# Optimization experiments

Measured on AMD Instinct MI355X. Metric: run time of the kernel, lower is better.

The kernel has to match this reference:

```python
import jax, jax.numpy as jnp
import numpy as np

N_RBF = 20
CUTOFF = 15.0
N_ATOMS, N_EDGES, D, H = 8192, 262144, 256, 256
D_PAIR = 2 * D + 1 + N_RBF  # 533


def setup_inputs() -> dict:
    key = jax.random.key(0)
    ks = jax.random.split(key, 10)
    s = 1.0 / np.sqrt(H).astype(np.float32)
    return {
        "x": jax.random.normal(ks[0], (N_ATOMS, D), jnp.float32),
        "d_ij": jax.random.uniform(ks[1], (N_EDGES,), jnp.float32, 0.5, CUTOFF),
        "idx_i": jnp.sort(jax.random.randint(ks[2], (N_EDGES,), 0, N_ATOMS)),
        "idx_j": jax.random.randint(ks[3], (N_EDGES,), 0, N_ATOMS),
        "W_in": jax.random.normal(ks[4], (D_PAIR, H), jnp.float32) / np.sqrt(D_PAIR).astype(np.float32),
        "b_in": jnp.zeros((H,), jnp.float32),
        "Ws": jax.random.normal(ks[5], (6, H, H), jnp.float32) * s,
        "bs": jnp.zeros((6, H), jnp.float32),
        "W_out": jax.random.normal(ks[6], (H, 1), jnp.float32) * s,
        "b_out": jnp.zeros((1,), jnp.float32),
    }


def _gaussian_rbf(d):
    # GaussianRBF(20, 15.0): offsets linspace(0, cutoff), width = grid spacing
    offsets = jnp.linspace(0.0, CUTOFF, N_RBF)
    width = offsets[1] - offsets[0]
    coeff = -0.5 / (width * width)
    diff = d[:, None] - offsets  # [E, N_RBF]
    return jnp.exp(coeff * diff * diff)


def reference(x, d_ij, idx_i, idx_j, W_in, b_in, Ws, bs, W_out, b_out):
    n_atoms = x.shape[0]
    rbf = _gaussian_rbf(d_ij)  # [E, 20]
    # per-pair representation: x_i | x_j | rbf(d_ij) | d_ij  -> [E, 533]
    pair = jnp.concatenate([x[idx_i], x[idx_j], rbf, d_ij[:, None]], axis=1)
    h = pair @ W_in + b_in  # pair_and_distance_transform -> [E, 256]
    # build_mlp(H, H, H, 5): 6 linears, SiLU after all but the last
    for l in range(6):
        h = h @ Ws[l] + bs[l]
        if l < 5:
            h = jax.nn.silu(h)
    # DeepSets aggregation: scatter-sum pair messages onto center atom i
    pooled = jax.ops.segment_sum(h, idx_i, num_segments=n_atoms)  # [N, 256]
    out = pooled @ W_out + b_out  # per-atom energy [N, 1]
    return out
```

## Files before the change

kernel.cpp:

```cpp
#include <hip/hip_runtime.h>


typedef _Float16 f16x8 __attribute__((ext_vector_type(8)));
typedef _Float16 f16x4 __attribute__((ext_vector_type(4)));
typedef __fp16   fp16v2 __attribute__((ext_vector_type(2)));
typedef float    f32x4 __attribute__((ext_vector_type(4)));
typedef unsigned int u32x4 __attribute__((ext_vector_type(4)));
typedef unsigned int u32x2 __attribute__((ext_vector_type(2)));

union H8 { f16x8 v; _Float16 h[8]; u32x4 u; };
union H4 { f16x4 v; u32x2 u; };
union H2 { fp16v2 h; unsigned int u; };

#define MFMA16(a, b, c) __builtin_amdgcn_mfma_f32_16x16x32_f16((a), (b), (c), 0, 0, 0)

#define LOG2E 1.44269504088896340736f

#define WS_WP   0u
#define WS_WPI  786432u
#define WS_WPJ  917504u
#define WS_WPR  1048576u
#define WS_XH   1064960u
#define WS_AP   5259264u
#define WS_BP   9453568u

__global__ __launch_bounds__(256) void k_prep(
    const float* __restrict__ x, const float* __restrict__ W_in,
    const float* __restrict__ Ws, const float* __restrict__ b_out,
    _Float16* __restrict__ wp, _Float16* __restrict__ wpi,
    _Float16* __restrict__ wpj, _Float16* __restrict__ wpr,
    _Float16* __restrict__ xh, float* __restrict__ out)
{
  int i = blockIdx.x * 256 + threadIdx.x;
  if (i < 2097152) { xh[i] = (_Float16)x[i]; return; }
  i -= 2097152;
  if (i < 393216) {
    int m = i >> 16, r = i & 65535;
    int j = r & 7, lane = (r >> 3) & 63, ks = (r >> 9) & 7, nt = (r >> 12) & 15;
    int k = ks * 32 + (lane >> 4) * 8 + j, n = nt * 16 + (lane & 15);
    wp[i] = (_Float16)Ws[(m * 256 + k) * 256 + n];
    return;
  }
  i -= 393216;
  if (i < 65536) {
    int j = i & 7, lane = (i >> 3) & 63, ks = (i >> 9) & 7, nt = (i >> 12) & 15;
    int k = ks * 32 + (lane >> 4) * 8 + j, n = nt * 16 + (lane & 15);
    wpi[i] = (_Float16)W_in[k * 256 + n];
    return;
  }
  i -= 65536;
  if (i < 65536) {
    int j = i & 7, lane = (i >> 3) & 63, ks = (i >> 9) & 7, nt = (i >> 12) & 15;
    int k = ks * 32 + (lane >> 4) * 8 + j, n = nt * 16 + (lane & 15);
    wpj[i] = (_Float16)W_in[(256 + k) * 256 + n];
    return;
  }
  i -= 65536;
  if (i < 8192) {
    int j = i & 7, lane = (i >> 3) & 63, nt = (i >> 9) & 15;
    int k = (lane >> 4) * 8 + j, n = nt * 16 + (lane & 15);
    float v = 0.0f;
    if (k < 20)       v = W_in[(512 + k) * 256 + n];
    else if (k == 20) v = W_in[532 * 256 + n];
    wpr[i] = (_Float16)v;
    return;
  }
  i -= 8192;
  if (i < 8192) out[i] = b_out[0];
}

__global__ __launch_bounds__(256) void k_atoms(
    const _Float16* __restrict__ xh,
    const _Float16* __restrict__ wpi, const _Float16* __restrict__ wpj,
    const float* __restrict__ b_in,
    _Float16* __restrict__ AP, _Float16* __restrict__ BP)
{
  const int tid = threadIdx.x;
  const int l = tid & 63, w = tid >> 6;
  const int g = l >> 4, c = l & 15;
  const int which = blockIdx.y;
  const _Float16* wpx = which ? wpj : wpi;
  _Float16* outp = which ? BP : AP;
  const int abase = blockIdx.x * 64;

  f32x4 acc[4][4];
#pragma unroll
  for (int nf = 0; nf < 4; ++nf)
#pragma unroll
    for (int at = 0; at < 4; ++at) acc[nf][at] = (f32x4)0.0f;

#pragma unroll
  for (int ks = 0; ks < 8; ++ks) {
    f16x8 a[4];
#pragma unroll
    for (int nf = 0; nf < 4; ++nf) {
      H8 t; t.u = *(const u32x4*)(wpx + (((w * 4 + nf) * 8 + ks) * 64 + l) * 8);
      a[nf] = t.v;
    }
#pragma unroll
    for (int at = 0; at < 4; ++at) {
      H8 b; b.u = *(const u32x4*)(xh + (abase + at * 16 + c) * 256 + ks * 32 + g * 8);
#pragma unroll
      for (int nf = 0; nf < 4; ++nf)
        acc[nf][at] = MFMA16(a[nf], b.v, acc[nf][at]);
    }
  }

#pragma unroll
  for (int nf = 0; nf < 4; ++nf) {
    const int n = w * 64 + nf * 16 + g * 4;
    f32x4 bias = (f32x4)0.0f;
    if (!which) bias = *(const f32x4*)(b_in + n);
#pragma unroll
    for (int at = 0; at < 4; ++at) {
      const int atom = abase + at * 16 + c;
      const f32x4 t = acc[nf][at] + bias;
      H2 lo, hi;
      lo.h = __builtin_amdgcn_cvt_pkrtz(t[0], t[1]);
      hi.h = __builtin_amdgcn_cvt_pkrtz(t[2], t[3]);
      u32x2 q; q[0] = lo.u; q[1] = hi.u;
      *(u32x2*)(outp + atom * 256 + n) = q;
    }
  }
}

__global__ __launch_bounds__(512, 2) void k_edges(
    const _Float16* __restrict__ AP, const _Float16* __restrict__ BP,
    const int* __restrict__ idx_i, const int* __restrict__ idx_j,
    const float* __restrict__ d_ij,
    const _Float16* __restrict__ wp, const _Float16* __restrict__ wpr,
    const float* __restrict__ bs, const float* __restrict__ W_out,
    float* __restrict__ out)
{
  __shared__ __align__(16) char hb[131072];
  __shared__ float d_lds[256];
  __shared__ int   ii_lds[256];
  __shared__ int   jj_lds[256];
  __shared__ float oacc[256];

  const int tid = threadIdx.x;
  const int l = tid & 63, w = tid >> 6;
  const int fg = w & 3, eg = w >> 2;
  const int g = l >> 4, c = l & 15;
  const int ebase = blockIdx.x * 256;
  const int nb = fg * 64;
  const int eb = eg * 128;
  const int sw = (c << 4) | ((c & 1) << 8);

  if (tid < 256) {
    ii_lds[tid] = idx_i[ebase + tid];
    jj_lds[tid] = idx_j[ebase + tid];
    d_lds[tid]  = d_ij[ebase + tid];
    oacc[tid]   = 0.0f;
  }
  __syncthreads();

  f32x4 acc[4][8];

  {
    const float STEP = 15.0f / 19.0f;
    const float C2 = (-0.5f / (STEP * STEP)) * LOG2E;
    f16x8 afr[4];
#pragma unroll
    for (int nf = 0; nf < 4; ++nf) {
      H8 t; t.u = *(const u32x4*)(wpr + ((fg * 4 + nf) * 64 + l) * 8);
      afr[nf] = t.v;
    }
#pragma unroll
    for (int et = 0; et < 8; ++et) {
      const float d = d_lds[eb + et * 16 + c];
      H8 bb;
#pragma unroll
      for (int j = 0; j < 8; ++j) {
        const int k = g * 8 + j;
        float v = 0.0f;
        if (k < 20)       { const float df = d - (float)k * STEP; v = __builtin_amdgcn_exp2f(C2 * df * df); }
        else if (k == 20) { v = d; }
        bb.h[j] = (_Float16)v;
      }
      const f32x4 z = (f32x4)0.0f;
#pragma unroll
      for (int nf = 0; nf < 4; ++nf)
        acc[nf][et] = MFMA16(afr[nf], bb.v, z);
    }
  }
#pragma unroll
  for (int nf = 0; nf < 4; ++nf) {
    const int n = nb + nf * 16 + g * 4;
    const int obase = n * 2;
#pragma unroll
    for (int et = 0; et < 8; ++et) {
      const int el = eb + et * 16 + c;
      H4 pa, pb, s;
      pa.u = *(const u32x2*)(AP + ii_lds[el] * 256 + n);
      pb.u = *(const u32x2*)(BP + jj_lds[el] * 256 + n);
      H2 lo, hi;
      lo.h = __builtin_amdgcn_cvt_pkrtz(acc[nf][et][0], acc[nf][et][1]);
      hi.h = __builtin_amdgcn_cvt_pkrtz(acc[nf][et][2], acc[nf][et][3]);
      s.u[0] = lo.u; s.u[1] = hi.u;
      s.v = s.v + pa.v + pb.v;
      *(u32x2*)(hb + el * 512 + (obase ^ sw)) = s.u;
    }
  }
  __syncthreads();

  auto mfma_layer = [&](const _Float16* wl, const float* brow) {
#pragma unroll
    for (int nf = 0; nf < 4; ++nf) {
      const f32x4 bias = *(const f32x4*)(brow + nb + nf * 16 + g * 4);
#pragma unroll
      for (int et = 0; et < 8; ++et) acc[nf][et] = bias;
    }
    __builtin_amdgcn_s_setprio(1);
#pragma unroll
    for (int ks = 0; ks < 8; ++ks) {
      f16x8 a[4];
#pragma unroll
      for (int nf = 0; nf < 4; ++nf) {
        H8 t; t.u = *(const u32x4*)(wl + (((fg * 4 + nf) * 8 + ks) * 64 + l) * 8);
        a[nf] = t.v;
      }
      const int o = (ks * 64 + g * 16) ^ sw;
#pragma unroll
      for (int et = 0; et < 8; ++et) {
        const int el = eb + et * 16 + c;
        H8 b; b.u = *(const u32x4*)(hb + el * 512 + o);
#pragma unroll
        for (int nf = 0; nf < 4; ++nf)
          acc[nf][et] = MFMA16(a[nf], b.v, acc[nf][et]);
      }
    }
    __builtin_amdgcn_s_setprio(0);
  };

#pragma unroll 1
  for (int ly = 0; ly < 5; ++ly) {
    mfma_layer(wp + ly * 65536, bs + ly * 256);
    __syncthreads();
#pragma unroll
    for (int nf = 0; nf < 4; ++nf) {
      const int n = nb + nf * 16 + g * 4;
      const int obase = n * 2;
#pragma unroll
      for (int et = 0; et < 8; ++et) {
        f32x4 v = acc[nf][et];
#pragma unroll
        for (int j = 0; j < 4; ++j) {
          const float e = __builtin_amdgcn_exp2f(v[j] * -LOG2E);
          v[j] = v[j] * __builtin_amdgcn_rcpf(1.0f + e);
        }
        const int el = eb + et * 16 + c;
        H2 lo, hi;
        lo.h = __builtin_amdgcn_cvt_pkrtz(v[0], v[1]);
        hi.h = __builtin_amdgcn_cvt_pkrtz(v[2], v[3]);
        u32x2 q; q[0] = lo.u; q[1] = hi.u;
        *(u32x2*)(hb + el * 512 + (obase ^ sw)) = q;
      }
    }
    __syncthreads();
  }

  mfma_layer(wp + 5 * 65536, bs + 5 * 256);
  float sum[8];
#pragma unroll
  for (int et = 0; et < 8; ++et) sum[et] = 0.0f;
#pragma unroll
  for (int nf = 0; nf < 4; ++nf) {
    const int n = nb + nf * 16 + g * 4;
    const f32x4 wo = *(const f32x4*)(W_out + n);
#pragma unroll
    for (int et = 0; et < 8; ++et) {
      const f32x4 v = acc[nf][et];
      sum[et] += v[0] * wo[0] + v[1] * wo[1] + v[2] * wo[2] + v[3] * wo[3];
    }
  }
#pragma unroll
  for (int et = 0; et < 8; ++et) {
    float s = sum[et];
    s += __shfl_xor(s, 16, 64);
    s += __shfl_xor(s, 32, 64);
    if (l < 16) atomicAdd(&oacc[eb + et * 16 + l], s);
  }
  __syncthreads();
  if (tid < 256) atomicAdd(out + ii_lds[tid], oacc[tid]);
}

extern "C" void kernel_launch(void* const* d_in, const int* in_sizes, int n_in,
                              void* d_out, int out_size, void* d_ws, size_t ws_size,
                              hipStream_t stream) {
  (void)in_sizes; (void)n_in; (void)out_size; (void)ws_size;
  const float* x     = (const float*)d_in[0];
  const float* d_ij  = (const float*)d_in[1];
  const int*   idx_i = (const int*)d_in[2];
  const int*   idx_j = (const int*)d_in[3];
  const float* W_in  = (const float*)d_in[4];
  const float* b_in  = (const float*)d_in[5];
  const float* Ws    = (const float*)d_in[6];
  const float* bs    = (const float*)d_in[7];
  const float* W_out = (const float*)d_in[8];
  const float* b_out = (const float*)d_in[9];
  float* out = (float*)d_out;
  char* ws = (char*)d_ws;

  _Float16* wp  = (_Float16*)(ws + WS_WP);
  _Float16* wpi = (_Float16*)(ws + WS_WPI);
  _Float16* wpj = (_Float16*)(ws + WS_WPJ);
  _Float16* wpr = (_Float16*)(ws + WS_WPR);
  _Float16* xh  = (_Float16*)(ws + WS_XH);
  _Float16* AP  = (_Float16*)(ws + WS_AP);
  _Float16* BP  = (_Float16*)(ws + WS_BP);

  hipLaunchKernelGGL(k_prep, dim3(10305), dim3(256), 0, stream,
                     x, W_in, Ws, b_out, wp, wpi, wpj, wpr, xh, out);
  hipLaunchKernelGGL(k_atoms, dim3(128, 2), dim3(256), 0, stream,
                     xh, wpi, wpj, b_in, AP, BP);
  hipLaunchKernelGGL(k_edges, dim3(1024), dim3(512), 0, stream,
                     AP, BP, idx_i, idx_j, d_ij, wp, wpr, bs, W_out, out);
}
```

Measured before the change: 297.0 us.

## Give each wave its own 32-edge slab covering all 256 output features

Reassigns work so each of the 8 waves owns 32 edges and computes all 256 hidden features for them, instead of a 4x2 split of features by edges across waves. Activations then stay in a per-wave LDS slab, which removes the cross-wave barrier between each layer's MFMA and its SiLU writeback. In exchange, weight fragments are reloaded from global/L2 for every k-step and every 16-feature tile with less reuse across edges, so each wave streams the whole weight matrix per layer instead of a quarter of it.

```diff
diff --git a/kernel.cpp b/kernel.cpp
--- a/kernel.cpp
+++ b/kernel.cpp
@@ -132,7 +132,7 @@
     const float* __restrict__ bs, const float* __restrict__ W_out,
     float* __restrict__ out)
 {
-  __shared__ __align__(16) char hb[131072];
+  __shared__ __align__(16) char hb[8][16384];
   __shared__ float d_lds[256];
   __shared__ int   ii_lds[256];
   __shared__ int   jj_lds[256];
@@ -140,12 +140,11 @@
 
   const int tid = threadIdx.x;
   const int l = tid & 63, w = tid >> 6;
-  const int fg = w & 3, eg = w >> 2;
   const int g = l >> 4, c = l & 15;
   const int ebase = blockIdx.x * 256;
-  const int nb = fg * 64;
-  const int eb = eg * 128;
+  const int web = w * 32;
   const int sw = (c << 4) | ((c & 1) << 8);
+  char* myh = hb[w];
 
   if (tid < 256) {
     ii_lds[tid] = idx_i[ebase + tid];
@@ -155,42 +154,40 @@
   }
   __syncthreads();
 
-  f32x4 acc[4][8];
+  f32x4 acc[16][2];
 
   {
     const float STEP = 15.0f / 19.0f;
     const float C2 = (-0.5f / (STEP * STEP)) * LOG2E;
-    f16x8 afr[4];
-#pragma unroll
-    for (int nf = 0; nf < 4; ++nf) {
-      H8 t; t.u = *(const u32x4*)(wpr + ((fg * 4 + nf) * 64 + l) * 8);
-      afr[nf] = t.v;
-    }
-#pragma unroll
-    for (int et = 0; et < 8; ++et) {
-      const float d = d_lds[eb + et * 16 + c];
-      H8 bb;
+    H8 bb[2];
+#pragma unroll
+    for (int et = 0; et < 2; ++et) {
+      const float d = d_lds[web + et * 16 + c];
 #pragma unroll
       for (int j = 0; j < 8; ++j) {
         const int k = g * 8 + j;
         float v = 0.0f;
         if (k < 20)       { const float df = d - (float)k * STEP; v = __builtin_amdgcn_exp2f(C2 * df * df); }
         else if (k == 20) { v = d; }
-        bb.h[j] = (_Float16)v;
+        bb[et].h[j] = (_Float16)v;
       }
-      const f32x4 z = (f32x4)0.0f;
-#pragma unroll
-      for (int nf = 0; nf < 4; ++nf)
-        acc[nf][et] = MFMA16(afr[nf], bb.v, z);
-    }
-  }
-#pragma unroll
-  for (int nf = 0; nf < 4; ++nf) {
-    const int n = nb + nf * 16 + g * 4;
+    }
+    const f32x4 z = (f32x4)0.0f;
+#pragma unroll
+    for (int nf = 0; nf < 16; ++nf) {
+      H8 t; t.u = *(const u32x4*)(wpr + (nf * 64 + l) * 8);
+      acc[nf][0] = MFMA16(t.v, bb[0].v, z);
+      acc[nf][1] = MFMA16(t.v, bb[1].v, z);
+    }
+  }
+#pragma unroll
+  for (int nf = 0; nf < 16; ++nf) {
+    const int n = nf * 16 + g * 4;
     const int obase = n * 2;
 #pragma unroll
-    for (int et = 0; et < 8; ++et) {
-      const int el = eb + et * 16 + c;
+    for (int et = 0; et < 2; ++et) {
+      const int el = web + et * 16 + c;
+      const int lel = et * 16 + c;
       H4 pa, pb, s;
       pa.u = *(const u32x2*)(AP + ii_lds[el] * 256 + n);
       pb.u = *(const u32x2*)(BP + jj_lds[el] * 256 + n);
@@ -199,35 +196,30 @@
       hi.h = __builtin_amdgcn_cvt_pkrtz(acc[nf][et][2], acc[nf][et][3]);
       s.u[0] = lo.u; s.u[1] = hi.u;
       s.v = s.v + pa.v + pb.v;
-      *(u32x2*)(hb + el * 512 + (obase ^ sw)) = s.u;
+      *(u32x2*)(myh + lel * 512 + (obase ^ sw)) = s.u;
     }
   }
   __syncthreads();
 
   auto mfma_layer = [&](const _Float16* wl, const float* brow) {
 #pragma unroll
-    for (int nf = 0; nf < 4; ++nf) {
-      const f32x4 bias = *(const f32x4*)(brow + nb + nf * 16 + g * 4);
-#pragma unroll
-      for (int et = 0; et < 8; ++et) acc[nf][et] = bias;
+    for (int nf = 0; nf < 16; ++nf) {
+      const f32x4 bias = *(const f32x4*)(brow + nf * 16 + g * 4);
+      acc[nf][0] = bias;
+      acc[nf][1] = bias;
     }
     __builtin_amdgcn_s_setprio(1);
 #pragma unroll
     for (int ks = 0; ks < 8; ++ks) {
-      f16x8 a[4];
-#pragma unroll
-      for (int nf = 0; nf < 4; ++nf) {
-        H8 t; t.u = *(const u32x4*)(wl + (((fg * 4 + nf) * 8 + ks) * 64 + l) * 8);
-        a[nf] = t.v;
-      }
       const int o = (ks * 64 + g * 16) ^ sw;
-#pragma unroll
-      for (int et = 0; et < 8; ++et) {
-        const int el = eb + et * 16 + c;
-        H8 b; b.u = *(const u32x4*)(hb + el * 512 + o);
-#pragma unroll
-        for (int nf = 0; nf < 4; ++nf)
-          acc[nf][et] = MFMA16(a[nf], b.v, acc[nf][et]);
+      H8 b0, b1;
+      b0.u = *(const u32x4*)(myh + c * 512 + o);
+      b1.u = *(const u32x4*)(myh + (16 + c) * 512 + o);
+#pragma unroll
+      for (int nf = 0; nf < 16; ++nf) {
+        H8 a; a.u = *(const u32x4*)(wl + ((nf * 8 + ks) * 64 + l) * 8);
+        acc[nf][0] = MFMA16(a.v, b0.v, acc[nf][0]);
+        acc[nf][1] = MFMA16(a.v, b1.v, acc[nf][1]);
       }
     }
     __builtin_amdgcn_s_setprio(0);
@@ -236,50 +228,46 @@
 #pragma unroll 1
   for (int ly = 0; ly < 5; ++ly) {
     mfma_layer(wp + ly * 65536, bs + ly * 256);
-    __syncthreads();
-#pragma unroll
-    for (int nf = 0; nf < 4; ++nf) {
-      const int n = nb + nf * 16 + g * 4;
-      const int obase = n * 2;
-#pragma unroll
-      for (int et = 0; et < 8; ++et) {
+#pragma unroll
+    for (int nf = 0; nf < 16; ++nf) {
+      const int obase = (nf * 16 + g * 4) * 2;
+#pragma unroll
+      for (int et = 0; et < 2; ++et) {
         f32x4 v = acc[nf][et];
 #pragma unroll
         for (int j = 0; j < 4; ++j) {
           const float e = __builtin_amdgcn_exp2f(v[j] * -LOG2E);
           v[j] = v[j] * __builtin_amdgcn_rcpf(1.0f + e);
         }
-        const int el = eb + et * 16 + c;
+        const int lel = et * 16 + c;
         H2 lo, hi;
         lo.h = __builtin_amdgcn_cvt_pkrtz(v[0], v[1]);
         hi.h = __builtin_amdgcn_cvt_pkrtz(v[2], v[3]);
         u32x2 q; q[0] = lo.u; q[1] = hi.u;
-        *(u32x2*)(hb + el * 512 + (obase ^ sw)) = q;
+        *(u32x2*)(myh + lel * 512 + (obase ^ sw)) = q;
       }
     }
     __syncthreads();
   }
 
   mfma_layer(wp + 5 * 65536, bs + 5 * 256);
-  float sum[8];
-#pragma unroll
-  for (int et = 0; et < 8; ++et) sum[et] = 0.0f;
-#pragma unroll
-  for (int nf = 0; nf < 4; ++nf) {
-    const int n = nb + nf * 16 + g * 4;
-    const f32x4 wo = *(const f32x4*)(W_out + n);
-#pragma unroll
-    for (int et = 0; et < 8; ++et) {
+  float sum[2];
+  sum[0] = 0.0f; sum[1] = 0.0f;
+#pragma unroll
+  for (int nf = 0; nf < 16; ++nf) {
+    const f32x4 wo = *(const f32x4*)(W_out + nf * 16 + g * 4);
+#pragma unroll
+    for (int et = 0; et < 2; ++et) {
       const f32x4 v = acc[nf][et];
       sum[et] += v[0] * wo[0] + v[1] * wo[1] + v[2] * wo[2] + v[3] * wo[3];
     }
   }
 #pragma unroll
-  for (int et = 0; et < 8; ++et) {
+  for (int et = 0; et < 2; ++et) {
     float s = sum[et];
     s += __shfl_xor(s, 16, 64);
     s += __shfl_xor(s, 32, 64);
-    if (l < 16) atomicAdd(&oacc[eb + et * 16 + l], s);
+    if (l < 16) atomicAdd(&oacc[web + et * 16 + l], s);
   }
   __syncthreads();
   if (tid < 256) atomicAdd(out + ii_lds[tid], oacc[tid]);
```

New measurement: 853.3 us. 2.87x slower.
